# Performance work log

Measured on AMD Instinct MI355X. Metric: run time of the kernel, lower is better.

The kernel has to match this reference:

```python
import jax, jax.numpy as jnp
import numpy as np

B, S, H, NH = 4, 1024, 1024, 16
HD = H // NH
CAUSAL_HEADS = 4
META_HEADS = NH // 4
CAUSAL_W = 0.7                      # cognitive_state['reasoning']['causal_active'] > 0.5 -> branch on
META_W = ((0.9 - 0.8) / 0.2) * 0.3  # awareness_level = 0.9 > 0.8 -> meta branch on, blend = 0.15


def _mha(xq, xkv, Win, bi, Wout, bout, nh):
    """torch nn.MultiheadAttention (batch_first) with packed in_proj [H, 3H]."""
    b, sq, h = xq.shape
    sk = xkv.shape[1]
    hd = h // nh
    q = (xq @ Win[:, :h] + bi[:h]).reshape(b, sq, nh, hd).transpose(0, 2, 1, 3)
    k = (xkv @ Win[:, h:2 * h] + bi[h:2 * h]).reshape(b, sk, nh, hd).transpose(0, 2, 1, 3)
    v = (xkv @ Win[:, 2 * h:] + bi[2 * h:]).reshape(b, sk, nh, hd).transpose(0, 2, 1, 3)
    scores = jnp.einsum('bhqd,bhkd->bhqk', q, k) / jnp.sqrt(jnp.asarray(hd, q.dtype))
    probs = jax.nn.softmax(scores, axis=-1)
    ctx = jnp.einsum('bhqk,bhkd->bhqd', probs, v)
    return ctx.transpose(0, 2, 1, 3).reshape(b, sq, h) @ Wout + bout


def _forward(hidden_states, cons_vec, Wq, bq, Wk, bk, Wv, bv, cg_W, cg_b, am_W, am_b,
             ca_Win, ca_bin, ca_Wout, ca_bout, mc_Win, mc_bin, mc_Wout, mc_bout, Wo, bo):
    b, s, h = hidden_states.shape
    q = (hidden_states @ Wq + bq).reshape(b, s, NH, HD).transpose(0, 2, 1, 3)
    k = (hidden_states @ Wk + bk).reshape(b, s, NH, HD).transpose(0, 2, 1, 3)
    v = (hidden_states @ Wv + bv).reshape(b, s, NH, HD).transpose(0, 2, 1, 3)
    scores = jnp.einsum('bhqd,bhkd->bhqk', q, k) / jnp.sqrt(jnp.asarray(HD, q.dtype))
    # consciousness-gated score modulation: sigmoid(gate(x) + awareness(cons_vec)) per (query, head)
    mod = jax.nn.sigmoid(hidden_states @ cg_W + cg_b + (cons_vec @ am_W + am_b))  # [B,S,NH]
    scores = scores * mod.transpose(0, 2, 1)[..., None]  # [B,NH,S,1] broadcast over keys
    probs = jax.nn.softmax(scores, axis=-1)
    ctx = jnp.einsum('bhqk,bhkd->bhqd', probs, v).transpose(0, 2, 1, 3).reshape(b, s, h)
    # causal MHA branch (active: causal_active=0.7 > 0.5)
    causal_ctx = _mha(hidden_states, hidden_states, ca_Win, ca_bin, ca_Wout, ca_bout, CAUSAL_HEADS)
    ctx = ctx * (1.0 - CAUSAL_W) + causal_ctx * CAUSAL_W
    # metacognitive MHA branch (active: awareness=0.9 > 0.8)
    meta_ctx = _mha(ctx, ctx, mc_Win, mc_bin, mc_Wout, mc_bout, META_HEADS)
    ctx = ctx * (1.0 - META_W) + meta_ctx * META_W
    return ctx @ Wo + bo


def setup_inputs() -> dict:
    key = jax.random.key(0)
    ks = jax.random.split(key, 16)
    sc = 0.02
    d = {
        'hidden_states': jax.random.normal(ks[0], (B, S, H), jnp.float32),
        'cons_vec': jax.random.uniform(ks[1], (16,), jnp.float32),
        'Wq': jax.random.normal(ks[2], (H, H), jnp.float32) * sc, 'bq': jnp.zeros((H,), jnp.float32),
        'Wk': jax.random.normal(ks[3], (H, H), jnp.float32) * sc, 'bk': jnp.zeros((H,), jnp.float32),
        'Wv': jax.random.normal(ks[4], (H, H), jnp.float32) * sc, 'bv': jnp.zeros((H,), jnp.float32),
        'cg_W': jax.random.normal(ks[5], (H, NH), jnp.float32) * sc, 'cg_b': jnp.zeros((NH,), jnp.float32),
        'am_W': jax.random.normal(ks[6], (16, NH), jnp.float32) * sc, 'am_b': jnp.zeros((NH,), jnp.float32),
        'ca_Win': jax.random.normal(ks[7], (H, 3 * H), jnp.float32) * sc, 'ca_bin': jnp.zeros((3 * H,), jnp.float32),
        'ca_Wout': jax.random.normal(ks[8], (H, H), jnp.float32) * sc, 'ca_bout': jnp.zeros((H,), jnp.float32),
        'mc_Win': jax.random.normal(ks[9], (H, 3 * H), jnp.float32) * sc, 'mc_bin': jnp.zeros((3 * H,), jnp.float32),
        'mc_Wout': jax.random.normal(ks[10], (H, H), jnp.float32) * sc, 'mc_bout': jnp.zeros((H,), jnp.float32),
        'Wo': jax.random.normal(ks[11], (H, H), jnp.float32) * sc, 'bo': jnp.zeros((H,), jnp.float32),
    }
    return d


def reference(hidden_states, cons_vec, Wq, bq, Wk, bk, Wv, bv, cg_W, cg_b, am_W, am_b,
              ca_Win, ca_bin, ca_Wout, ca_bout, mc_Win, mc_bin, mc_Wout, mc_bout, Wo, bo):
    return _forward(hidden_states, cons_vec, Wq, bq, Wk, bk, Wv, bv, cg_W, cg_b, am_W, am_b,
                    ca_Win, ca_bin, ca_Wout, ca_bout, mc_Win, mc_bin, mc_Wout, mc_bout, Wo, bo)
```

## Files before the change

### kernel.cpp

```cpp
#include <hip/hip_runtime.h>
#include <stdint.h>

typedef unsigned short u16;
typedef __attribute__((ext_vector_type(8))) short short8;
typedef __attribute__((ext_vector_type(4))) float f32x4;

#define MFMA16(a,b,c) __builtin_amdgcn_mfma_f32_16x16x32_bf16((a),(b),(c),0,0,0)

__device__ __forceinline__ u16 f2bf(float f) {
  union { float f; uint32_t u; } v; v.f = f;
  uint32_t r = v.u + 0x7FFFu + ((v.u >> 16) & 1u);
  return (u16)(r >> 16);
}
__device__ __forceinline__ float bf2f(uint32_t u) {
  union { uint32_t i; float f; } v; v.i = u << 16; return v.f;
}
__device__ __forceinline__ void async_copy16(void* lds, const void* g) {
  __builtin_amdgcn_global_load_lds(
      (const __attribute__((address_space(1))) uint32_t*)g,
      (__attribute__((address_space(3))) uint32_t*)lds, 16, 0, 0);
}

__device__ __forceinline__ void transpose8x8(uint32_t r[4], int lane8) {
  uint32_t a0, a1, a2, a3;
  a0 = __shfl_xor(r[0], 4); a1 = __shfl_xor(r[1], 4);
  a2 = __shfl_xor(r[2], 4); a3 = __shfl_xor(r[3], 4);
  if (lane8 & 4) { r[0] = a2; r[1] = a3; } else { r[2] = a0; r[3] = a1; }
  a0 = __shfl_xor(r[0], 2); a1 = __shfl_xor(r[1], 2);
  a2 = __shfl_xor(r[2], 2); a3 = __shfl_xor(r[3], 2);
  if (lane8 & 2) { r[0] = a1; r[2] = a3; } else { r[1] = a0; r[3] = a2; }
  a0 = __shfl_xor(r[0], 1); a1 = __shfl_xor(r[1], 1);
  a2 = __shfl_xor(r[2], 1); a3 = __shfl_xor(r[3], 1);
  uint32_t sel = (lane8 & 1) ? 0x03020706u : 0x05040100u;
  r[0] = __builtin_amdgcn_perm(a0, r[0], sel);
  r[1] = __builtin_amdgcn_perm(a1, r[1], sel);
  r[2] = __builtin_amdgcn_perm(a2, r[2], sel);
  r[3] = __builtin_amdgcn_perm(a3, r[3], sel);
}

__global__ __launch_bounds__(256) void castmod_kernel(
    const float* __restrict__ X, u16* __restrict__ Xbf,
    const float* __restrict__ cgW, const float* __restrict__ cgb,
    const float* __restrict__ cons, const float* __restrict__ amW,
    const float* __restrict__ amb, float* __restrict__ modp) {
  __shared__ float xs[1024];
  __shared__ float part[16][16];
  __shared__ float am[16];
  int row = blockIdx.x, t = threadIdx.x;
  {
    float4 v = ((const float4*)(X + (size_t)row * 1024))[t];
    xs[t * 4 + 0] = v.x; xs[t * 4 + 1] = v.y; xs[t * 4 + 2] = v.z; xs[t * 4 + 3] = v.w;
    uint2 o;
    o.x = (uint32_t)f2bf(v.x) | ((uint32_t)f2bf(v.y) << 16);
    o.y = (uint32_t)f2bf(v.z) | ((uint32_t)f2bf(v.w) << 16);
    ((uint2*)Xbf)[(size_t)row * 256 + t] = o;
  }
  if (t < 16) {
    float a = amb[t];
#pragma unroll
    for (int i = 0; i < 16; i++) a += cons[i] * amW[i * 16 + t];
    am[t] = a;
  }
  __syncthreads();
  int h = t & 15, ch = t >> 4;
  float p = 0.f;
#pragma unroll 8
  for (int k = ch * 64; k < ch * 64 + 64; k++) p += xs[k] * cgW[k * 16 + h];
  part[ch][h] = p;
  __syncthreads();
  if (t < 16) {
    float s = cgb[t] + am[t];
#pragma unroll
    for (int c = 0; c < 16; c++) s += part[c][t];
    int b = row >> 10, si = row & 1023;
    modp[((size_t)(b * 16 + t)) * 1024 + si] = 0.125f / (1.f + __expf(-s));
  }
}

struct TBatch { const float* src[6]; u16* dst[6]; };
__global__ __launch_bounds__(256) void transpose_cast_batch(
    TBatch p, int rows, int cols) {
  __shared__ float tile[32][33];
  const float* __restrict__ in = p.src[blockIdx.z];
  u16* __restrict__ out = p.dst[blockIdx.z];
  int c0 = blockIdx.x * 32, r0 = blockIdx.y * 32;
  int tx = threadIdx.x, ty = threadIdx.y;
#pragma unroll
  for (int j = 0; j < 4; j++)
    tile[ty + j * 8][tx] = in[(size_t)(r0 + ty + j * 8) * cols + c0 + tx];
  __syncthreads();
#pragma unroll
  for (int j = 0; j < 4; j++)
    out[(size_t)(c0 + ty + j * 8) * rows + r0 + tx] = f2bf(tile[tx][ty + j * 8]);
}

__global__ void pack_bias3(const float* __restrict__ a, const float* __restrict__ b,
                           const float* __restrict__ c, float* __restrict__ o) {
  int i = blockIdx.x * 256 + threadIdx.x;
  o[i] = (i < 1024) ? a[i] : (i < 2048 ? b[i - 1024] : c[i - 2048]);
}

__global__ void zero_f32(float* __restrict__ p) {
  p[blockIdx.x * 256 + threadIdx.x] = 0.f;
}

template <int OUT_F32, int HAS_EXTRA, int BN>
__global__ __launch_bounds__(256, 3) void gemm_bt(
    const u16* __restrict__ A, const u16* __restrict__ Bt,
    const float* __restrict__ bias, const u16* __restrict__ extra,
    float alpha, float beta, void* __restrict__ Cout, int M, int N, int K) {
  constexpr int NJ = BN / 32;
  __shared__ u16 As[128 * 64];
  __shared__ u16 Bs[BN * 64];
  const int t = threadIdx.x;
  const int w = t >> 6, l = t & 63, lm = l & 15, lg = l >> 4;
  const int wm = w & 1, wn = w >> 1;
  const int m0 = blockIdx.y * 128, n0 = blockIdx.x * BN;
  const int rl = l >> 3, gsrc8 = ((l & 7) ^ (rl & 7)) * 8;
  const f32x4 fzero = {0.f, 0.f, 0.f, 0.f};
  f32x4 acc[4][NJ];
#pragma unroll
  for (int i = 0; i < 4; i++)
#pragma unroll
    for (int j = 0; j < NJ; j++) acc[i][j] = fzero;

  for (int kt = 0; kt < K; kt += 64) {
    __syncthreads();
#pragma unroll
    for (int c = 0; c < 4; c++) {
      int rb = c * 32 + w * 8;
      async_copy16(&As[rb * 64], A + (size_t)(m0 + rb + rl) * K + kt + gsrc8);
    }
#pragma unroll
    for (int c = 0; c < BN / 32; c++) {
      int rb = c * 32 + w * 8;
      async_copy16(&Bs[rb * 64], Bt + (size_t)(n0 + rb + rl) * K + kt + gsrc8);
    }
    __syncthreads();
#pragma unroll
    for (int kk = 0; kk < 2; kk++) {
      short8 af[4], bf[NJ];
      const int gph = ((kk * 4 + lg) ^ (lm & 7)) * 8;
#pragma unroll
      for (int i = 0; i < 4; i++)
        af[i] = *(const short8*)&As[(wm * 64 + i * 16 + lm) * 64 + gph];
#pragma unroll
      for (int j = 0; j < NJ; j++)
        bf[j] = *(const short8*)&Bs[(wn * (BN / 2) + j * 16 + lm) * 64 + gph];
#pragma unroll
      for (int i = 0; i < 4; i++)
#pragma unroll
        for (int j = 0; j < NJ; j++) acc[i][j] = MFMA16(af[i], bf[j], acc[i][j]);
    }
  }
#pragma unroll
  for (int i = 0; i < 4; i++) {
    int row0 = m0 + wm * 64 + i * 16 + lg * 4;
#pragma unroll
    for (int j = 0; j < NJ; j++) {
      int col = n0 + wn * (BN / 2) + j * 16 + lm;
      float bc = bias[col];
#pragma unroll
      for (int r = 0; r < 4; r++) {
        size_t idx = (size_t)(row0 + r) * N + col;
        float v = acc[i][j][r] + bc;
        if constexpr (HAS_EXTRA) v = alpha * v + beta * bf2f(extra[idx]);
        if constexpr (OUT_F32) ((float*)Cout)[idx] = v;
        else ((u16*)Cout)[idx] = f2bf(v);
      }
    }
  }
}

__global__ __launch_bounds__(256, 3) void gemm_vt(
    const u16* __restrict__ A, const u16* __restrict__ Bt,
    const float* __restrict__ bias, u16* __restrict__ Vtb) {
  constexpr int K = 1024;
  __shared__ u16 As[128 * 64];
  __shared__ u16 Bs[128 * 64];
  const int t = threadIdx.x;
  const int w = t >> 6, l = t & 63, lm = l & 15, lg = l >> 4;
  const int wm = w & 1, wn = w >> 1;
  const int m0 = blockIdx.y * 128, n0 = blockIdx.x * 128;
  const int rl = l >> 3, gsrc8 = ((l & 7) ^ (rl & 7)) * 8;
  const f32x4 fzero = {0.f, 0.f, 0.f, 0.f};
  f32x4 acc[4][4];
#pragma unroll
  for (int i = 0; i < 4; i++)
#pragma unroll
    for (int j = 0; j < 4; j++) acc[i][j] = fzero;

  for (int kt = 0; kt < K; kt += 64) {
    __syncthreads();
#pragma unroll
    for (int c = 0; c < 4; c++) {
      int rb = c * 32 + w * 8;
      async_copy16(&As[rb * 64], A + (size_t)(m0 + rb + rl) * K + kt + gsrc8);
      async_copy16(&Bs[rb * 64], Bt + (size_t)(n0 + rb + rl) * K + kt + gsrc8);
    }
    __syncthreads();
#pragma unroll
    for (int kk = 0; kk < 2; kk++) {
      short8 af[4], bf[4];
      const int gph = ((kk * 4 + lg) ^ (lm & 7)) * 8;
#pragma unroll
      for (int i = 0; i < 4; i++)
        af[i] = *(const short8*)&As[(wm * 64 + i * 16 + lm) * 64 + gph];
#pragma unroll
      for (int j = 0; j < 4; j++)
        bf[j] = *(const short8*)&Bs[(wn * 64 + j * 16 + lm) * 64 + gph];
#pragma unroll
      for (int i = 0; i < 4; i++)
#pragma unroll
        for (int j = 0; j < 4; j++) acc[i][j] = MFMA16(af[i], bf[j], acc[i][j]);
    }
  }
#pragma unroll
  for (int i = 0; i < 4; i++) {
    int row0 = m0 + wm * 64 + i * 16 + lg * 4;
    int b = row0 >> 10, q0 = row0 & 1023;
#pragma unroll
    for (int j = 0; j < 4; j++) {
      int col = n0 + wn * 64 + j * 16 + lm;
      float bc = bias[col];
      int z = b * 4 + (col >> 8), d = col & 255;
      union { u16 pk[4]; uint2 v; } u;
#pragma unroll
      for (int r = 0; r < 4; r++) u.pk[r] = f2bf(acc[i][j][r] + bc);
      *(uint2*)&Vtb[((size_t)z * 256 + d) * 1024 + q0] = u.v;
    }
  }
}

__global__ __launch_bounds__(256, 3) void gemm_qk_exp(
    const u16* __restrict__ qkv, u16* __restrict__ P, float* __restrict__ lrow,
    float scale) {
  constexpr int W3 = 3072;
  __shared__ u16 As[128 * 64];
  __shared__ u16 Bs[128 * 64];
  const int t = threadIdx.x;
  const int w = t >> 6, l = t & 63, lm = l & 15, lg = l >> 4;
  const int wm = w & 1, wn = w >> 1;
  const int z = blockIdx.z, b = z >> 2, h = z & 3;
  const int m0 = blockIdx.y * 128, n0 = blockIdx.x * 128;
  const u16* Abase = qkv + ((size_t)b << 10) * W3 + h * 256;
  const u16* Bbase = qkv + ((size_t)b << 10) * W3 + 1024 + h * 256;
  const int rl = l >> 3, gsrc8 = ((l & 7) ^ (rl & 7)) * 8;
  const f32x4 fzero = {0.f, 0.f, 0.f, 0.f};
  f32x4 acc[4][4];
#pragma unroll
  for (int i = 0; i < 4; i++)
#pragma unroll
    for (int j = 0; j < 4; j++) acc[i][j] = fzero;

#pragma unroll
  for (int kt = 0; kt < 256; kt += 64) {
    __syncthreads();
#pragma unroll
    for (int c = 0; c < 4; c++) {
      int rb = c * 32 + w * 8;
      async_copy16(&As[rb * 64], Abase + (size_t)(m0 + rb + rl) * W3 + kt + gsrc8);
      async_copy16(&Bs[rb * 64], Bbase + (size_t)(n0 + rb + rl) * W3 + kt + gsrc8);
    }
    __syncthreads();
#pragma unroll
    for (int kk = 0; kk < 2; kk++) {
      short8 af[4], bf[4];
      const int gph = ((kk * 4 + lg) ^ (lm & 7)) * 8;
#pragma unroll
      for (int i = 0; i < 4; i++)
        af[i] = *(const short8*)&As[(wm * 64 + i * 16 + lm) * 64 + gph];
#pragma unroll
      for (int j = 0; j < 4; j++)
        bf[j] = *(const short8*)&Bs[(wn * 64 + j * 16 + lm) * 64 + gph];
#pragma unroll
      for (int i = 0; i < 4; i++)
#pragma unroll
        for (int j = 0; j < 4; j++) acc[i][j] = MFMA16(af[i], bf[j], acc[i][j]);
    }
  }
  u16* Pz = P + ((size_t)z << 20);
#pragma unroll
  for (int i = 0; i < 4; i++) {
    int row0 = m0 + wm * 64 + i * 16 + lg * 4;
    float rsum[4] = {0.f, 0.f, 0.f, 0.f};
#pragma unroll
    for (int j = 0; j < 4; j++) {
      int col = n0 + wn * 64 + j * 16 + lm;
#pragma unroll
      for (int r = 0; r < 4; r++) {
        float p = __expf(acc[i][j][r] * scale);
        rsum[r] += p;
        Pz[(size_t)(row0 + r) * 1024 + col] = f2bf(p);
      }
    }
#pragma unroll
    for (int r = 0; r < 4; r++) {
      float s = rsum[r];
#pragma unroll
      for (int sh = 1; sh <= 8; sh <<= 1) s += __shfl_xor(s, sh);
      if (lm == 0) atomicAdd(&lrow[(z << 10) + row0 + r], s);
    }
  }
}

__global__ __launch_bounds__(256, 3) void gemm_pv(
    const u16* __restrict__ P, const u16* __restrict__ Vtb,
    const float* __restrict__ lrow, u16* __restrict__ outp) {
  constexpr int K = 1024, BN = 64, NJ = 2;
  __shared__ u16 As[128 * 64];
  __shared__ u16 Bs[BN * 64];
  const int t = threadIdx.x;
  const int w = t >> 6, l = t & 63, lm = l & 15, lg = l >> 4;
  const int wm = w & 1, wn = w >> 1;
  const int z = blockIdx.z, b = z >> 2, h = z & 3;
  const int m0 = blockIdx.y * 128, n0 = blockIdx.x * BN;
  const u16* Abase = P + ((size_t)z << 20);
  const u16* Bbase = Vtb + ((size_t)z << 18);
  const int rl = l >> 3, gsrc8 = ((l & 7) ^ (rl & 7)) * 8;
  const f32x4 fzero = {0.f, 0.f, 0.f, 0.f};
  f32x4 acc[4][NJ];
#pragma unroll
  for (int i = 0; i < 4; i++)
#pragma unroll
    for (int j = 0; j < NJ; j++) acc[i][j] = fzero;

  for (int kt = 0; kt < K; kt += 64) {
    __syncthreads();
#pragma unroll
    for (int c = 0; c < 4; c++) {
      int rb = c * 32 + w * 8;
      async_copy16(&As[rb * 64], Abase + (size_t)(m0 + rb + rl) * K + kt + gsrc8);
    }
#pragma unroll
    for (int c = 0; c < BN / 32; c++) {
      int rb = c * 32 + w * 8;
      async_copy16(&Bs[rb * 64], Bbase + (size_t)(n0 + rb + rl) * K + kt + gsrc8);
    }
    __syncthreads();
#pragma unroll
    for (int kk = 0; kk < 2; kk++) {
      short8 af[4], bf[NJ];
      const int gph = ((kk * 4 + lg) ^ (lm & 7)) * 8;
#pragma unroll
      for (int i = 0; i < 4; i++)
        af[i] = *(const short8*)&As[(wm * 64 + i * 16 + lm) * 64 + gph];
#pragma unroll
      for (int j = 0; j < NJ; j++)
        bf[j] = *(const short8*)&Bs[(wn * (BN / 2) + j * 16 + lm) * 64 + gph];
#pragma unroll
      for (int i = 0; i < 4; i++)
#pragma unroll
        for (int j = 0; j < NJ; j++) acc[i][j] = MFMA16(af[i], bf[j], acc[i][j]);
    }
  }
#pragma unroll
  for (int i = 0; i < 4; i++) {
    int row0 = m0 + wm * 64 + i * 16 + lg * 4;
    float invl[4];
#pragma unroll
    for (int r = 0; r < 4; r++) invl[r] = 1.f / lrow[(z << 10) + row0 + r];
#pragma unroll
    for (int j = 0; j < NJ; j++) {
      int col = n0 + wn * (BN / 2) + j * 16 + lm;
#pragma unroll
      for (int r = 0; r < 4; r++)
        outp[(size_t)((b << 10) + row0 + r) * 1024 + h * 256 + col] =
            f2bf(acc[i][j][r] * invl[r]);
    }
  }
}

__global__ __launch_bounds__(256, 3) void flash_attn64(
    const u16* __restrict__ qkv, const float* __restrict__ modp,
    u16* __restrict__ outp) {
  constexpr int S = 1024, W3 = 3072, HD = 64, BKV = 128;
  constexpr int NKD = 2, NT = 8, ND = 4, NKP = 4, KC = 4;
  constexpr int VSTR = 136, PSTR = 136;

  __shared__ u16 Ks[BKV * HD];
  __shared__ u16 Vt[HD * VSTR];
  __shared__ u16 Ps[64 * PSTR];

  const int t = threadIdx.x, w = t >> 6, l = t & 63, lm = l & 15, lg = l >> 4;
  const int bid = blockIdx.x;
  const int rest = bid >> 3;
  const int q0 = (rest & 15) * 64;
  const int bh = (bid & 7) + 8 * (rest >> 4);
  const int b = bh >> 4, h = bh & 15;
  const size_t rowbase = (size_t)b * S;

  const int oc = t >> 3, kvo = t & 7;
  const int sd0 = (oc & 7) * 8;
  const int skvg = (oc >> 3) * 8;

  short8 qf[NKD];
  {
    const u16* qp = qkv + (rowbase + q0 + w * 16 + lm) * W3 + h * HD + lg * 8;
#pragma unroll
    for (int d = 0; d < NKD; d++) qf[d] = *(const short8*)(qp + d * 32);
  }
  float rs[4];
#pragma unroll
  for (int r = 0; r < 4; r++)
    rs[r] = modp[(size_t)bh * S + q0 + w * 16 + lg * 4 + r];

  float lsum[4] = {0.f, 0.f, 0.f, 0.f};
  const f32x4 fzero = {0.f, 0.f, 0.f, 0.f};
  f32x4 oacc[ND];
#pragma unroll
  for (int d = 0; d < ND; d++) oacc[d] = fzero;

  for (int kb = 0; kb < S; kb += BKV) {
    __syncthreads();
#pragma unroll
    for (int c = 0; c < 4; c++) {
      int rb = c * 32 + w * 8;
      int row = rb + (l >> 3);
      int gsrc = ((l & 7) ^ (row & 7)) * 8;
      async_copy16(&Ks[rb * HD],
                   qkv + (rowbase + kb + row) * W3 + 1024 + h * HD + gsrc);
    }
#pragma unroll
    for (int c = 0; c < KC; c++) {
      int kv = c * 32 + skvg + kvo;
      union { short8 s; uint32_t u[4]; } vv, vo;
      vv.s = *(const short8*)(qkv + (rowbase + kb + kv) * W3 + 2048 + h * HD + sd0);
      uint32_t r[4] = {vv.u[0], vv.u[1], vv.u[2], vv.u[3]};
      transpose8x8(r, kvo);
      vo.u[0] = r[0]; vo.u[1] = r[1]; vo.u[2] = r[2]; vo.u[3] = r[3];
      *(short8*)&Vt[(sd0 + kvo) * VSTR + c * 32 + skvg] = vo.s;
    }
    __syncthreads();

    f32x4 sacc[NT];
#pragma unroll
    for (int n = 0; n < NT; n++) sacc[n] = fzero;
#pragma unroll
    for (int n = 0; n < NT; n++) {
      int krow = n * 16 + lm;
#pragma unroll
      for (int d = 0; d < NKD; d++) {
        int g = d * 4 + lg;
        short8 kf = *(const short8*)&Ks[krow * HD + ((g ^ (krow & 7)) * 8)];
        sacc[n] = MFMA16(qf[d], kf, sacc[n]);
      }
    }
#pragma unroll
    for (int n = 0; n < NT; n++) {
#pragma unroll
      for (int r = 0; r < 4; r++) {
        float p = __expf(sacc[n][r] * rs[r]);
        lsum[r] += p;
        Ps[(w * 16 + lg * 4 + r) * PSTR + n * 16 + lm] = f2bf(p);
      }
    }
#pragma unroll
    for (int ks = 0; ks < NKP; ks++) {
      short8 pf = *(const short8*)&Ps[(w * 16 + lm) * PSTR + ks * 32 + lg * 8];
#pragma unroll
      for (int d = 0; d < ND; d++) {
        short8 vf = *(const short8*)&Vt[(d * 16 + lm) * VSTR + ks * 32 + lg * 8];
        oacc[d] = MFMA16(pf, vf, oacc[d]);
      }
    }
  }
  float invl[4];
#pragma unroll
  for (int r = 0; r < 4; r++) {
    float s = lsum[r];
#pragma unroll
    for (int sh = 1; sh <= 8; sh <<= 1) s += __shfl_xor(s, sh);
    invl[r] = 1.f / s;
  }
#pragma unroll
  for (int d = 0; d < ND; d++) {
    int col = h * HD + d * 16 + lm;
#pragma unroll
    for (int r = 0; r < 4; r++) {
      int row = q0 + w * 16 + lg * 4 + r;
      outp[(rowbase + row) * 1024 + col] = f2bf(oacc[d][r] * invl[r]);
    }
  }
}

extern "C" void kernel_launch(void* const* d_in, const int* in_sizes, int n_in,
                              void* d_out, int out_size, void* d_ws, size_t ws_size,
                              hipStream_t stream) {
  (void)in_sizes; (void)n_in; (void)out_size; (void)ws_size;
  const float* X      = (const float*)d_in[0];
  const float* cons   = (const float*)d_in[1];
  const float* Wq     = (const float*)d_in[2];  const float* bq     = (const float*)d_in[3];
  const float* Wk     = (const float*)d_in[4];  const float* bk     = (const float*)d_in[5];
  const float* Wv     = (const float*)d_in[6];  const float* bv     = (const float*)d_in[7];
  const float* cgW    = (const float*)d_in[8];  const float* cgb    = (const float*)d_in[9];
  const float* amW    = (const float*)d_in[10]; const float* amb    = (const float*)d_in[11];
  const float* caWin  = (const float*)d_in[12]; const float* cabin  = (const float*)d_in[13];
  const float* caWout = (const float*)d_in[14]; const float* cabout = (const float*)d_in[15];
  const float* mcWin  = (const float*)d_in[16]; const float* mcbin  = (const float*)d_in[17];
  const float* mcWout = (const float*)d_in[18]; const float* mcbout = (const float*)d_in[19];
  const float* Wo     = (const float*)d_in[20]; const float* bo     = (const float*)d_in[21];

  char* ws = (char*)d_ws;
  size_t off = 0;
  auto alloc = [&](size_t bytes) -> void* {
    void* p = ws + off; off += (bytes + 255) & ~(size_t)255; return p;
  };
  u16*    Xbf     = (u16*)alloc((size_t)4096 * 1024 * 2);
  u16*    WqkvT   = (u16*)alloc((size_t)3072 * 1024 * 2);
  u16*    caWinT  = (u16*)alloc((size_t)3072 * 1024 * 2);
  u16*    mcWinT  = (u16*)alloc((size_t)3072 * 1024 * 2);
  u16*    caWoutT = (u16*)alloc((size_t)1024 * 1024 * 2);
  u16*    mcWoutT = (u16*)alloc((size_t)1024 * 1024 * 2);
  u16*    WoT     = (u16*)alloc((size_t)1024 * 1024 * 2);
  float*  bqkv    = (float*)alloc(3072 * 4);
  float*  modb    = (float*)alloc((size_t)64 * 1024 * 4);
  u16*    big0    = (u16*)alloc((size_t)4096 * 3072 * 2);
  u16*    actx    = (u16*)alloc((size_t)4096 * 1024 * 2);
  u16*    ctxm    = (u16*)alloc((size_t)4096 * 1024 * 2);
  u16*    ctx1    = (u16*)alloc((size_t)4096 * 1024 * 2);
  u16*    Pbuf    = (u16*)alloc((size_t)16 * 1024 * 1024 * 2);
  u16*    Vtb     = (u16*)alloc((size_t)16 * 256 * 1024 * 2);
  float*  lbuf    = (float*)alloc((size_t)2 * 16384 * 4);
  float*  l_ca    = lbuf;
  float*  l_mc    = lbuf + 16384;
  u16*    mctx    = ctxm;
  u16*    ctx2    = actx;

  castmod_kernel<<<4096, 256, 0, stream>>>(X, Xbf, cgW, cgb, cons, amW, amb, modb);
  {
    TBatch b6;
    b6.src[0] = Wq;     b6.dst[0] = WqkvT;
    b6.src[1] = Wk;     b6.dst[1] = WqkvT + (size_t)1024 * 1024;
    b6.src[2] = Wv;     b6.dst[2] = WqkvT + (size_t)2048 * 1024;
    b6.src[3] = caWout; b6.dst[3] = caWoutT;
    b6.src[4] = mcWout; b6.dst[4] = mcWoutT;
    b6.src[5] = Wo;     b6.dst[5] = WoT;
    transpose_cast_batch<<<dim3(32, 32, 6), dim3(32, 8), 0, stream>>>(b6, 1024, 1024);
    TBatch b2;
    b2.src[0] = caWin;  b2.dst[0] = caWinT;
    b2.src[1] = mcWin;  b2.dst[1] = mcWinT;
    b2.src[2] = b2.src[3] = b2.src[4] = b2.src[5] = nullptr;
    b2.dst[2] = b2.dst[3] = b2.dst[4] = b2.dst[5] = nullptr;
    transpose_cast_batch<<<dim3(96, 32, 2), dim3(32, 8), 0, stream>>>(b2, 1024, 3072);
  }
  pack_bias3<<<12, 256, 0, stream>>>(bq, bk, bv, bqkv);
  zero_f32<<<128, 256, 0, stream>>>(lbuf);

  gemm_bt<0, 0, 128><<<dim3(16, 32), 256, 0, stream>>>(Xbf, caWinT, cabin, nullptr, 0.f, 0.f,
                                                       big0, 4096, 3072, 1024);
  gemm_vt<<<dim3(8, 32), 256, 0, stream>>>(Xbf, caWinT + (size_t)2048 * 1024,
                                           cabin + 2048, Vtb);
  gemm_qk_exp<<<dim3(8, 8, 16), 256, 0, stream>>>(big0, Pbuf, l_ca, 1.f / 16.f);
  gemm_pv<<<dim3(4, 8, 16), 256, 0, stream>>>(Pbuf, Vtb, l_ca, actx);

  gemm_bt<0, 0, 128><<<dim3(24, 32), 256, 0, stream>>>(Xbf, WqkvT, bqkv, nullptr, 0.f, 0.f,
                                                       big0, 4096, 3072, 1024);
  flash_attn64<<<1024, 256, 0, stream>>>(big0, modb, ctxm);

  gemm_bt<0, 1, 64><<<dim3(16, 32), 256, 0, stream>>>(actx, caWoutT, cabout, ctxm, 0.7f, 0.3f,
                                                      ctx1, 4096, 1024, 1024);

  gemm_bt<0, 0, 128><<<dim3(16, 32), 256, 0, stream>>>(ctx1, mcWinT, mcbin, nullptr, 0.f, 0.f,
                                                       big0, 4096, 3072, 1024);
  gemm_vt<<<dim3(8, 32), 256, 0, stream>>>(ctx1, mcWinT + (size_t)2048 * 1024,
                                           mcbin + 2048, Vtb);
  gemm_qk_exp<<<dim3(8, 8, 16), 256, 0, stream>>>(big0, Pbuf, l_mc, 1.f / 16.f);
  gemm_pv<<<dim3(4, 8, 16), 256, 0, stream>>>(Pbuf, Vtb, l_mc, mctx);

  gemm_bt<0, 1, 64><<<dim3(16, 32), 256, 0, stream>>>(mctx, mcWoutT, mcbout, ctx1, 0.15f, 0.85f,
                                                      ctx2, 4096, 1024, 1024);
  gemm_bt<1, 0, 64><<<dim3(16, 32), 256, 0, stream>>>(ctx2, WoT, bo, nullptr, 0.f, 0.f,
                                                      d_out, 4096, 1024, 1024);
}
```

Before: 482.4 us.

## Fuse input projections into one wide GEMM, merge prep kernels, enlarge flash query tile

Merges the weight transpose/cast, bias packing and lbuf zeroing into a single prep launch. The causal-branch in-proj (Q,K,V^T) and the main QKV projection now run as one 6144-wide GEMM over the shared input, with column-range-dependent epilogues, so the X operand is loaded once and fewer GEMM launches are needed. The redundant second V GEMM is gone. The flash attention kernel now handles 128 queries per block (two 64-row sub-tiles reusing each K/V tile) with launch bounds lowered to 2 waves per EU. This trades higher register and LDS use and fewer blocks for better K/V reuse.

```diff
diff --git a/kernel.cpp b/kernel.cpp
--- a/kernel.cpp
+++ b/kernel.cpp
@@ -77,31 +77,43 @@
   }
 }
 
-struct TBatch { const float* src[6]; u16* dst[6]; };
-__global__ __launch_bounds__(256) void transpose_cast_batch(
-    TBatch p, int rows, int cols) {
-  __shared__ float tile[32][33];
-  const float* __restrict__ in = p.src[blockIdx.z];
-  u16* __restrict__ out = p.dst[blockIdx.z];
-  int c0 = blockIdx.x * 32, r0 = blockIdx.y * 32;
-  int tx = threadIdx.x, ty = threadIdx.y;
-#pragma unroll
-  for (int j = 0; j < 4; j++)
-    tile[ty + j * 8][tx] = in[(size_t)(r0 + ty + j * 8) * cols + c0 + tx];
-  __syncthreads();
-#pragma unroll
-  for (int j = 0; j < 4; j++)
-    out[(size_t)(c0 + ty + j * 8) * rows + r0 + tx] = f2bf(tile[tx][ty + j * 8]);
-}
-
-__global__ void pack_bias3(const float* __restrict__ a, const float* __restrict__ b,
-                           const float* __restrict__ c, float* __restrict__ o) {
-  int i = blockIdx.x * 256 + threadIdx.x;
-  o[i] = (i < 1024) ? a[i] : (i < 2048 ? b[i - 1024] : c[i - 2048]);
-}
-
-__global__ void zero_f32(float* __restrict__ p) {
-  p[blockIdx.x * 256 + threadIdx.x] = 0.f;
+struct PrepArgs {
+  const float* src[12];
+  u16* dst[12];
+  int sstride[12];
+  const float* cabin; const float* bq; const float* bk; const float* bv;
+  float* biasBig; float* lbuf;
+};
+__global__ __launch_bounds__(256) void prep_weights(PrepArgs p) {
+  int z = blockIdx.z;
+  int tx = threadIdx.x & 31, ty = threadIdx.x >> 5;
+  if (z < 12) {
+    __shared__ float tile[32][33];
+    const float* __restrict__ in = p.src[z];
+    u16* __restrict__ out = p.dst[z];
+    int sstr = p.sstride[z];
+    int c0 = blockIdx.x * 32, r0 = blockIdx.y * 32;
+#pragma unroll
+    for (int j = 0; j < 4; j++)
+      tile[ty + j * 8][tx] = in[(size_t)(r0 + ty + j * 8) * sstr + c0 + tx];
+    __syncthreads();
+#pragma unroll
+    for (int j = 0; j < 4; j++)
+      out[(size_t)(c0 + ty + j * 8) * 1024 + r0 + tx] = f2bf(tile[tx][ty + j * 8]);
+  } else {
+    int id = blockIdx.y * 32 + blockIdx.x, t = threadIdx.x;
+    if (id < 24) {
+      int i = id * 256 + t;
+      float v;
+      if (i < 3072) v = p.cabin[i];
+      else if (i < 4096) v = p.bq[i - 3072];
+      else if (i < 5120) v = p.bk[i - 4096];
+      else v = p.bv[i - 5120];
+      p.biasBig[i] = v;
+    } else if (id < 152) {
+      p.lbuf[(id - 24) * 256 + t] = 0.f;
+    }
+  }
 }
 
 template <int OUT_F32, int HAS_EXTRA, int BN>
@@ -172,9 +184,10 @@
   }
 }
 
-__global__ __launch_bounds__(256, 3) void gemm_vt(
-    const u16* __restrict__ A, const u16* __restrict__ Bt,
-    const float* __restrict__ bias, u16* __restrict__ Vtb) {
+__global__ __launch_bounds__(256, 3) void gemm_in3(
+    const u16* __restrict__ A, const u16* __restrict__ BtBig,
+    const float* __restrict__ bias, u16* __restrict__ qkOut,
+    u16* __restrict__ Vtb, u16* __restrict__ qkvm) {
   constexpr int K = 1024;
   __shared__ u16 As[128 * 64];
   __shared__ u16 Bs[128 * 64];
@@ -196,7 +209,7 @@
     for (int c = 0; c < 4; c++) {
       int rb = c * 32 + w * 8;
       async_copy16(&As[rb * 64], A + (size_t)(m0 + rb + rl) * K + kt + gsrc8);
-      async_copy16(&Bs[rb * 64], Bt + (size_t)(n0 + rb + rl) * K + kt + gsrc8);
+      async_copy16(&Bs[rb * 64], BtBig + (size_t)(n0 + rb + rl) * K + kt + gsrc8);
     }
     __syncthreads();
 #pragma unroll
@@ -218,24 +231,34 @@
 #pragma unroll
   for (int i = 0; i < 4; i++) {
     int row0 = m0 + wm * 64 + i * 16 + lg * 4;
-    int b = row0 >> 10, q0 = row0 & 1023;
 #pragma unroll
     for (int j = 0; j < 4; j++) {
       int col = n0 + wn * 64 + j * 16 + lm;
       float bc = bias[col];
-      int z = b * 4 + (col >> 8), d = col & 255;
-      union { u16 pk[4]; uint2 v; } u;
-#pragma unroll
-      for (int r = 0; r < 4; r++) u.pk[r] = f2bf(acc[i][j][r] + bc);
-      *(uint2*)&Vtb[((size_t)z * 256 + d) * 1024 + q0] = u.v;
+      if (col < 2048) {
+#pragma unroll
+        for (int r = 0; r < 4; r++)
+          qkOut[(size_t)(row0 + r) * 2048 + col] = f2bf(acc[i][j][r] + bc);
+      } else if (col < 3072) {
+        int b = row0 >> 10, q0 = row0 & 1023;
+        int z = b * 4 + ((col - 2048) >> 8), d = (col - 2048) & 255;
+        union { u16 pk[4]; uint2 v; } u;
+#pragma unroll
+        for (int r = 0; r < 4; r++) u.pk[r] = f2bf(acc[i][j][r] + bc);
+        *(uint2*)&Vtb[((size_t)z * 256 + d) * 1024 + q0] = u.v;
+      } else {
+#pragma unroll
+        for (int r = 0; r < 4; r++)
+          qkvm[(size_t)(row0 + r) * 3072 + col - 3072] = f2bf(acc[i][j][r] + bc);
+      }
     }
   }
 }
 
 __global__ __launch_bounds__(256, 3) void gemm_qk_exp(
-    const u16* __restrict__ qkv, u16* __restrict__ P, float* __restrict__ lrow,
+    const u16* __restrict__ qk, u16* __restrict__ P, float* __restrict__ lrow,
     float scale) {
-  constexpr int W3 = 3072;
+  constexpr int QKS = 2048;
   __shared__ u16 As[128 * 64];
   __shared__ u16 Bs[128 * 64];
   const int t = threadIdx.x;
@@ -243,8 +266,8 @@
   const int wm = w & 1, wn = w >> 1;
   const int z = blockIdx.z, b = z >> 2, h = z & 3;
   const int m0 = blockIdx.y * 128, n0 = blockIdx.x * 128;
-  const u16* Abase = qkv + ((size_t)b << 10) * W3 + h * 256;
-  const u16* Bbase = qkv + ((size_t)b << 10) * W3 + 1024 + h * 256;
+  const u16* Abase = qk + ((size_t)b << 10) * QKS + h * 256;
+  const u16* Bbase = qk + ((size_t)b << 10) * QKS + 1024 + h * 256;
   const int rl = l >> 3, gsrc8 = ((l & 7) ^ (rl & 7)) * 8;
   const f32x4 fzero = {0.f, 0.f, 0.f, 0.f};
   f32x4 acc[4][4];
@@ -259,8 +282,8 @@
 #pragma unroll
     for (int c = 0; c < 4; c++) {
       int rb = c * 32 + w * 8;
-      async_copy16(&As[rb * 64], Abase + (size_t)(m0 + rb + rl) * W3 + kt + gsrc8);
-      async_copy16(&Bs[rb * 64], Bbase + (size_t)(n0 + rb + rl) * W3 + kt + gsrc8);
+      async_copy16(&As[rb * 64], Abase + (size_t)(m0 + rb + rl) * QKS + kt + gsrc8);
+      async_copy16(&Bs[rb * 64], Bbase + (size_t)(n0 + rb + rl) * QKS + kt + gsrc8);
     }
     __syncthreads();
 #pragma unroll
@@ -371,7 +394,7 @@
   }
 }
 
-__global__ __launch_bounds__(256, 3) void flash_attn64(
+__global__ __launch_bounds__(256, 2) void flash_attn64(
     const u16* __restrict__ qkv, const float* __restrict__ modp,
     u16* __restrict__ outp) {
   constexpr int S = 1024, W3 = 3072, HD = 64, BKV = 128;
@@ -380,13 +403,13 @@
 
   __shared__ u16 Ks[BKV * HD];
   __shared__ u16 Vt[HD * VSTR];
-  __shared__ u16 Ps[64 * PSTR];
+  __shared__ u16 Ps[128 * PSTR];
 
   const int t = threadIdx.x, w = t >> 6, l = t & 63, lm = l & 15, lg = l >> 4;
   const int bid = blockIdx.x;
   const int rest = bid >> 3;
-  const int q0 = (rest & 15) * 64;
-  const int bh = (bid & 7) + 8 * (rest >> 4);
+  const int q0 = (rest & 7) * 128;
+  const int bh = (bid & 7) + 8 * (rest >> 3);
   const int b = bh >> 4, h = bh & 15;
   const size_t rowbase = (size_t)b * S;
 
@@ -394,22 +417,25 @@
   const int sd0 = (oc & 7) * 8;
   const int skvg = (oc >> 3) * 8;
 
-  short8 qf[NKD];
-  {
-    const u16* qp = qkv + (rowbase + q0 + w * 16 + lm) * W3 + h * HD + lg * 8;
-#pragma unroll
-    for (int d = 0; d < NKD; d++) qf[d] = *(const short8*)(qp + d * 32);
-  }
-  float rs[4];
-#pragma unroll
-  for (int r = 0; r < 4; r++)
-    rs[r] = modp[(size_t)bh * S + q0 + w * 16 + lg * 4 + r];
-
-  float lsum[4] = {0.f, 0.f, 0.f, 0.f};
+  short8 qf[2][NKD];
+  float rs[2][4];
+#pragma unroll
+  for (int qs = 0; qs < 2; qs++) {
+    const u16* qp = qkv + (rowbase + q0 + qs * 64 + w * 16 + lm) * W3 + h * HD + lg * 8;
+#pragma unroll
+    for (int d = 0; d < NKD; d++) qf[qs][d] = *(const short8*)(qp + d * 32);
+#pragma unroll
+    for (int r = 0; r < 4; r++)
+      rs[qs][r] = modp[(size_t)bh * S + q0 + qs * 64 + w * 16 + lg * 4 + r];
+  }
+
+  float lsum[2][4] = {{0.f, 0.f, 0.f, 0.f}, {0.f, 0.f, 0.f, 0.f}};
   const f32x4 fzero = {0.f, 0.f, 0.f, 0.f};
-  f32x4 oacc[ND];
-#pragma unroll
-  for (int d = 0; d < ND; d++) oacc[d] = fzero;
+  f32x4 oacc[2][ND];
+#pragma unroll
+  for (int qs = 0; qs < 2; qs++)
+#pragma unroll
+    for (int d = 0; d < ND; d++) oacc[qs][d] = fzero;
 
   for (int kb = 0; kb < S; kb += BKV) {
     __syncthreads();
@@ -433,53 +459,62 @@
     }
     __syncthreads();
 
-    f32x4 sacc[NT];
-#pragma unroll
-    for (int n = 0; n < NT; n++) sacc[n] = fzero;
-#pragma unroll
-    for (int n = 0; n < NT; n++) {
-      int krow = n * 16 + lm;
-#pragma unroll
-      for (int d = 0; d < NKD; d++) {
-        int g = d * 4 + lg;
-        short8 kf = *(const short8*)&Ks[krow * HD + ((g ^ (krow & 7)) * 8)];
-        sacc[n] = MFMA16(qf[d], kf, sacc[n]);
+#pragma unroll
+    for (int qs = 0; qs < 2; qs++) {
+      f32x4 sacc[NT];
+#pragma unroll
+      for (int n = 0; n < NT; n++) sacc[n] = fzero;
+#pragma unroll
+      for (int n = 0; n < NT; n++) {
+        int krow = n * 16 + lm;
+#pragma unroll
+        for (int d = 0; d < NKD; d++) {
+          int g = d * 4 + lg;
+          short8 kf = *(const short8*)&Ks[krow * HD + ((g ^ (krow & 7)) * 8)];
+          sacc[n] = MFMA16(qf[qs][d], kf, sacc[n]);
+        }
       }
-    }
-#pragma unroll
-    for (int n = 0; n < NT; n++) {
+#pragma unroll
+      for (int n = 0; n < NT; n++) {
+#pragma unroll
+        for (int r = 0; r < 4; r++) {
+          float p = __expf(sacc[n][r] * rs[qs][r]);
+          lsum[qs][r] += p;
+          Ps[(qs * 64 + w * 16 + lg * 4 + r) * PSTR + n * 16 + lm] = f2bf(p);
+        }
+      }
+    }
+#pragma unroll
+    for (int qs = 0; qs < 2; qs++) {
+#pragma unroll
+      for (int ks = 0; ks < NKP; ks++) {
+        short8 pf = *(const short8*)&Ps[(qs * 64 + w * 16 + lm) * PSTR + ks * 32 + lg * 8];
+#pragma unroll
+        for (int d = 0; d < ND; d++) {
+          short8 vf = *(const short8*)&Vt[(d * 16 + lm) * VSTR + ks * 32 + lg * 8];
+          oacc[qs][d] = MFMA16(pf, vf, oacc[qs][d]);
+        }
+      }
+    }
+  }
+#pragma unroll
+  for (int qs = 0; qs < 2; qs++) {
+    float invl[4];
+#pragma unroll
+    for (int r = 0; r < 4; r++) {
+      float s = lsum[qs][r];
+#pragma unroll
+      for (int sh = 1; sh <= 8; sh <<= 1) s += __shfl_xor(s, sh);
+      invl[r] = 1.f / s;
+    }
+#pragma unroll
+    for (int d = 0; d < ND; d++) {
+      int col = h * HD + d * 16 + lm;
 #pragma unroll
       for (int r = 0; r < 4; r++) {
-        float p = __expf(sacc[n][r] * rs[r]);
-        lsum[r] += p;
-        Ps[(w * 16 + lg * 4 + r) * PSTR + n * 16 + lm] = f2bf(p);
+        int row = q0 + qs * 64 + w * 16 + lg * 4 + r;
+        outp[(rowbase + row) * 1024 + col] = f2bf(oacc[qs][d][r] * invl[r]);
       }
-    }
-#pragma unroll
-    for (int ks = 0; ks < NKP; ks++) {
-      short8 pf = *(const short8*)&Ps[(w * 16 + lm) * PSTR + ks * 32 + lg * 8];
-#pragma unroll
-      for (int d = 0; d < ND; d++) {
-        short8 vf = *(const short8*)&Vt[(d * 16 + lm) * VSTR + ks * 32 + lg * 8];
-        oacc[d] = MFMA16(pf, vf, oacc[d]);
-      }
-    }
-  }
-  float invl[4];
-#pragma unroll
-  for (int r = 0; r < 4; r++) {
-    float s = lsum[r];
-#pragma unroll
-    for (int sh = 1; sh <= 8; sh <<= 1) s += __shfl_xor(s, sh);
-    invl[r] = 1.f / s;
-  }
-#pragma unroll
-  for (int d = 0; d < ND; d++) {
-    int col = h * HD + d * 16 + lm;
-#pragma unroll
-    for (int r = 0; r < 4; r++) {
-      int row = q0 + w * 16 + lg * 4 + r;
-      outp[(rowbase + row) * 1024 + col] = f2bf(oacc[d][r] * invl[r]);
     }
   }
 }
@@ -507,15 +542,15 @@
     void* p = ws + off; off += (bytes + 255) & ~(size_t)255; return p;
   };
   u16*    Xbf     = (u16*)alloc((size_t)4096 * 1024 * 2);
-  u16*    WqkvT   = (u16*)alloc((size_t)3072 * 1024 * 2);
-  u16*    caWinT  = (u16*)alloc((size_t)3072 * 1024 * 2);
+  u16*    BtBig   = (u16*)alloc((size_t)6144 * 1024 * 2);
   u16*    mcWinT  = (u16*)alloc((size_t)3072 * 1024 * 2);
   u16*    caWoutT = (u16*)alloc((size_t)1024 * 1024 * 2);
   u16*    mcWoutT = (u16*)alloc((size_t)1024 * 1024 * 2);
   u16*    WoT     = (u16*)alloc((size_t)1024 * 1024 * 2);
-  float*  bqkv    = (float*)alloc(3072 * 4);
+  float*  biasBig = (float*)alloc(6144 * 4);
   float*  modb    = (float*)alloc((size_t)64 * 1024 * 4);
-  u16*    big0    = (u16*)alloc((size_t)4096 * 3072 * 2);
+  u16*    caQK    = (u16*)alloc((size_t)4096 * 2048 * 2);
+  u16*    qkvm    = (u16*)alloc((size_t)4096 * 3072 * 2);
   u16*    actx    = (u16*)alloc((size_t)4096 * 1024 * 2);
   u16*    ctxm    = (u16*)alloc((size_t)4096 * 1024 * 2);
   u16*    ctx1    = (u16*)alloc((size_t)4096 * 1024 * 2);
@@ -524,50 +559,41 @@
   float*  lbuf    = (float*)alloc((size_t)2 * 16384 * 4);
   float*  l_ca    = lbuf;
   float*  l_mc    = lbuf + 16384;
+  u16*    mcQK    = caQK;
   u16*    mctx    = ctxm;
   u16*    ctx2    = actx;
 
   castmod_kernel<<<4096, 256, 0, stream>>>(X, Xbf, cgW, cgb, cons, amW, amb, modb);
   {
-    TBatch b6;
-    b6.src[0] = Wq;     b6.dst[0] = WqkvT;
-    b6.src[1] = Wk;     b6.dst[1] = WqkvT + (size_t)1024 * 1024;
-    b6.src[2] = Wv;     b6.dst[2] = WqkvT + (size_t)2048 * 1024;
-    b6.src[3] = caWout; b6.dst[3] = caWoutT;
-    b6.src[4] = mcWout; b6.dst[4] = mcWoutT;
-    b6.src[5] = Wo;     b6.dst[5] = WoT;
-    transpose_cast_batch<<<dim3(32, 32, 6), dim3(32, 8), 0, stream>>>(b6, 1024, 1024);
-    TBatch b2;
-    b2.src[0] = caWin;  b2.dst[0] = caWinT;
-    b2.src[1] = mcWin;  b2.dst[1] = mcWinT;
-    b2.src[2] = b2.src[3] = b2.src[4] = b2.src[5] = nullptr;
-    b2.dst[2] = b2.dst[3] = b2.dst[4] = b2.dst[5] = nullptr;
-    transpose_cast_batch<<<dim3(96, 32, 2), dim3(32, 8), 0, stream>>>(b2, 1024, 3072);
-  }
-  pack_bias3<<<12, 256, 0, stream>>>(bq, bk, bv, bqkv);
-  zero_f32<<<128, 256, 0, stream>>>(lbuf);
-
-  gemm_bt<0, 0, 128><<<dim3(16, 32), 256, 0, stream>>>(Xbf, caWinT, cabin, nullptr, 0.f, 0.f,
-                                                       big0, 4096, 3072, 1024);
-  gemm_vt<<<dim3(8, 32), 256, 0, stream>>>(Xbf, caWinT + (size_t)2048 * 1024,
-                                           cabin + 2048, Vtb);
-  gemm_qk_exp<<<dim3(8, 8, 16), 256, 0, stream>>>(big0, Pbuf, l_ca, 1.f / 16.f);
+    PrepArgs pa;
+    for (int s = 0; s < 3; s++) {
+      pa.src[s] = caWin + s * 1024; pa.dst[s] = BtBig + (size_t)s * 1024 * 1024;
+      pa.sstride[s] = 3072;
+    }
+    pa.src[3] = Wq; pa.dst[3] = BtBig + (size_t)3072 * 1024; pa.sstride[3] = 1024;
+    pa.src[4] = Wk; pa.dst[4] = BtBig + (size_t)4096 * 1024; pa.sstride[4] = 1024;
+    pa.src[5] = Wv; pa.dst[5] = BtBig + (size_t)5120 * 1024; pa.sstride[5] = 1024;
+    for (int s = 0; s < 3; s++) {
+      pa.src[6 + s] = mcWin + s * 1024; pa.dst[6 + s] = mcWinT + (size_t)s * 1024 * 1024;
+      pa.sstride[6 + s] = 3072;
+    }
+    pa.src[9]  = caWout; pa.dst[9]  = caWoutT; pa.sstride[9]  = 1024;
+    pa.src[10] = mcWout; pa.dst[10] = mcWoutT; pa.sstride[10] = 1024;
+    pa.src[11] = Wo;     pa.dst[11] = WoT;     pa.sstride[11] = 1024;
+    pa.cabin = cabin; pa.bq = bq; pa.bk = bk; pa.bv = bv;
+    pa.biasBig = biasBig; pa.lbuf = lbuf;
+    prep_weights<<<dim3(32, 32, 13), 256, 0, stream>>>(pa);
+  }
+
+  gemm_in3<<<dim3(48, 32), 256, 0, stream>>>(Xbf, BtBig, biasBig, caQK, Vtb, qkvm);
+  gemm_qk_exp<<<dim3(8, 8, 16), 256, 0, stream>>>(caQK, Pbuf, l_ca, 1.f / 16.f);
   gemm_pv<<<dim3(4, 8, 16), 256, 0, stream>>>(Pbuf, Vtb, l_ca, actx);
-
-  gemm_bt<0, 0, 128><<<dim3(24, 32), 256, 0, stream>>>(Xbf, WqkvT, bqkv, nullptr, 0.f, 0.f,
-                                                       big0, 4096, 3072, 1024);
-  flash_attn64<<<1024, 256, 0, stream>>>(big0, modb, ctxm);
-
+  flash_attn64<<<512, 256, 0, stream>>>(qkvm, modb, ctxm);
   gemm_bt<0, 1, 64><<<dim3(16, 32), 256, 0, stream>>>(actx, caWoutT, cabout, ctxm, 0.7f, 0.3f,
                                                       ctx1, 4096, 1024, 1024);
-
-  gemm_bt<0, 0, 128><<<dim3(16, 32), 256, 0, stream>>>(ctx1, mcWinT, mcbin, nullptr, 0.f, 0.f,
-                                                       big0, 4096, 3072, 1024);
-  gemm_vt<<<dim3(8, 32), 256, 0, stream>>>(ctx1, mcWinT + (size_t)2048 * 1024,
-                                           mcbin + 2048, Vtb);
-  gemm_qk_exp<<<dim3(8, 8, 16), 256, 0, stream>>>(big0, Pbuf, l_mc, 1.f / 16.f);
+  gemm_in3<<<dim3(24, 32), 256, 0, stream>>>(ctx1, mcWinT, mcbin, mcQK, Vtb, qkvm );
+  gemm_qk_exp<<<dim3(8, 8, 16), 256, 0, stream>>>(mcQK, Pbuf, l_mc, 1.f / 16.f);
   gemm_pv<<<dim3(4, 8, 16), 256, 0, stream>>>(Pbuf, Vtb, l_mc, mctx);
-
   gemm_bt<0, 1, 64><<<dim3(16, 32), 256, 0, stream>>>(mctx, mcWoutT, mcbout, ctx1, 0.15f, 0.85f,
                                                       ctx2, 4096, 1024, 1024);
   gemm_bt<1, 0, 64><<<dim3(16, 32), 256, 0, stream>>>(ctx2, WoT, bo, nullptr, 0.f, 0.f,
```

After: 442.6 us. 1.09x faster.
